# Kernel optimization log

Measured on AMD Instinct MI355X. Metric: run time of the kernel, lower is better.

The kernel has to match this reference:

```python
import jax, jax.numpy as jnp
import numpy as np

N_NODES = 100000
N_EDGES = 1600000


def gcn_conv(x, src, dst, w, W, b, n_nodes):
    # PyG GCNConv: linear -> add self-loops (weight 1) -> symmetric norm -> scatter-add -> bias
    h = x @ W  # [N, out]
    loop = jnp.arange(n_nodes, dtype=src.dtype)
    s = jnp.concatenate([src, loop])
    d = jnp.concatenate([dst, loop])
    ew = jnp.concatenate([w, jnp.ones((n_nodes,), dtype=w.dtype)])
    deg = jax.ops.segment_sum(ew, d, num_segments=n_nodes)  # weighted in-degree (incl. self-loop)
    dis = jnp.where(deg > 0, jax.lax.rsqrt(deg), 0.0)
    norm = dis[s] * ew * dis[d]  # [E+N]
    msgs = norm[:, None] * h[s]  # gather source features, scale per edge
    out = jax.ops.segment_sum(msgs, d, num_segments=n_nodes)  # scatter-add at destinations
    return out + b


def setup_inputs() -> dict:
    key = jax.random.key(0)
    ks = jax.random.split(key, 6)
    x = jax.random.normal(ks[0], (N_NODES, 128), dtype=jnp.float32)
    edge_index = jax.random.randint(ks[1], (2, N_EDGES), 0, N_NODES, dtype=jnp.int32)
    edge_weight = jax.random.uniform(ks[2], (N_EDGES,), dtype=jnp.float32)
    W1 = jax.random.normal(ks[3], (128, 64), dtype=jnp.float32) * (1.0 / np.sqrt(128))
    b1 = jnp.zeros((64,), dtype=jnp.float32)
    W2 = jax.random.normal(ks[4], (64, 16), dtype=jnp.float32) * (1.0 / np.sqrt(64))
    b2 = jnp.zeros((16,), dtype=jnp.float32)
    return {"x": x, "edge_index": edge_index, "edge_weight": edge_weight,
            "W1": W1, "b1": b1, "W2": W2, "b2": b2}


def reference(x, edge_index, edge_weight, W1, b1, W2, b2):
    src, dst = edge_index[0], edge_index[1]
    x_emb = gcn_conv(x, src, dst, edge_weight, W1, b1, N_NODES)
    h = jax.nn.relu(x_emb)  # dropout is identity in eval mode
    out = gcn_conv(h, src, dst, edge_weight, W2, b2, N_NODES)
    return (out, x_emb)
```

## Files before the change

kernel.cpp:

```cpp
#include <hip/hip_runtime.h>

#define NN 100000
#define NE 1600000
#define BSH 7
#define BSZ 128
#define NBKT 782
#define CAP 2560
#define NPB 256
#define EPB 6250

typedef unsigned short u16;
typedef unsigned int   u32;
typedef unsigned long long u64;
typedef __attribute__((ext_vector_type(8))) __bf16 bf16x8;
typedef __attribute__((ext_vector_type(4))) float  f32x4;

__device__ __forceinline__ float bf2f(u16 u) {
    union { u32 i; float f; } v; v.i = ((u32)u) << 16; return v.f;
}
__device__ __forceinline__ u16 f2bf(float f) {
    union { float f; u32 i; } v; v.f = f;
    u32 u = v.i;
    u += 0x7FFFu + ((u >> 16) & 1);
    return (u16)(u >> 16);
}
__device__ __forceinline__ float bfLO(u32 p) { return __uint_as_float(p << 16); }
__device__ __forceinline__ float bfHI(u32 p) { return __uint_as_float(p & 0xffff0000u); }
__device__ __forceinline__ u64 nt_load_u64(const uint2* p) {
    return __builtin_nontemporal_load((const u64*)p);
}

__global__ __launch_bounds__(256) void k_wpack(const float* __restrict__ W1,
                                               const float* __restrict__ W2,
                                               bf16x8* __restrict__ wp1,
                                               bf16x8* __restrict__ wp2,
                                               int* __restrict__ cursor,
                                               int* __restrict__ gctr) {
    int t = threadIdx.x;
    #pragma unroll
    for (int s = 0; s < 4; ++s) {
        int idx = s * 256 + t;
        int q = idx >> 6, l = idx & 63;
        int kb = q >> 2, ct = q & 3;
        int k0 = kb * 32 + ((l >> 4) * 8);
        int c  = ct * 16 + (l & 15);
        bf16x8 v;
        #pragma unroll
        for (int i = 0; i < 8; ++i) v[i] = (__bf16)W1[(k0 + i) * 64 + c];
        wp1[idx] = v;
    }
    if (t < 128) {
        int q = t >> 6, l = t & 63;
        int k0 = q * 32 + ((l >> 4) * 8);
        int c  = l & 15;
        bf16x8 v;
        #pragma unroll
        for (int i = 0; i < 8; ++i) v[i] = (__bf16)W2[(k0 + i) * 16 + c];
        wp2[t] = v;
    }
    for (int i = t; i < NBKT; i += 256) cursor[i] = i * CAP;
    if (t == 0) *gctr = 0;
}

__global__ __launch_bounds__(1024) void k_part(const int* __restrict__ src,
                                               const int* __restrict__ dst,
                                               const float* __restrict__ w,
                                               int* __restrict__ cursor,
                                               uint2* __restrict__ rec) {
    __shared__ uint2 sedge[EPB];
    __shared__ u16   sbkt[EPB];
    __shared__ int   cnt[NBKT];
    __shared__ int   lstart[NBKT];
    __shared__ int   gbase[NBKT];
    __shared__ int   scanbuf[1024];
    int tid = threadIdx.x;
    int e0  = blockIdx.x * EPB;

    for (int i = tid; i < NBKT; i += 1024) cnt[i] = 0;
    __syncthreads();
    for (int j = tid; j < EPB; j += 1024)
        atomicAdd(&cnt[dst[e0 + j] >> BSH], 1);
    __syncthreads();
    int v = (tid < NBKT) ? cnt[tid] : 0;
    scanbuf[tid] = v;
    __syncthreads();
    #pragma unroll
    for (int off = 1; off < 1024; off <<= 1) {
        int add = (tid >= off) ? scanbuf[tid - off] : 0;
        __syncthreads();
        scanbuf[tid] += add;
        __syncthreads();
    }
    if (tid < NBKT) lstart[tid] = scanbuf[tid] - v;
    __syncthreads();
    for (int i = tid; i < NBKT; i += 1024) {
        int c = cnt[i];
        gbase[i] = c ? atomicAdd(&cursor[i], c) : 0;
        cnt[i] = 0;
    }
    __syncthreads();
    for (int j = tid; j < EPB; j += 1024) {
        int e  = e0 + j;
        int d  = dst[e];
        int bk = d >> BSH;
        int slot = lstart[bk] + atomicAdd(&cnt[bk], 1);
        sedge[slot] = make_uint2(__float_as_uint(w[e]),
                                 ((u32)src[e] << BSH) | (u32)(d & (BSZ - 1)));
        sbkt[slot]  = (u16)bk;
    }
    __syncthreads();
    for (int j = tid; j < EPB; j += 1024) {
        int bk   = sbkt[j];
        int dest = gbase[bk] + (j - lstart[bk]);
        rec[dest] = sedge[j];
    }
}

__global__ __launch_bounds__(512) void k_build(const int* __restrict__ cursor,
                                               const uint2* __restrict__ rec,
                                               uint2* __restrict__ rec2,
                                               float* __restrict__ dis,
                                               int2* __restrict__ rowinfo,
                                               int* __restrict__ gctr) {
    __shared__ float dw[BSZ];
    __shared__ int   cnt[BSZ];
    __shared__ int   base[BSZ];
    __shared__ int   scn[BSZ];
    __shared__ float disl[BSZ];
    __shared__ int   sh_gbase;
    int b = blockIdx.x, tid = threadIdx.x;
    int s = b * CAP;
    int total = cursor[b] - s;
    if (tid < BSZ) { dw[tid] = 1.0f; cnt[tid] = 0; }
    if (tid == 0) sh_gbase = atomicAdd(gctr, total);
    __syncthreads();
    for (int j = tid; j < total; j += 512) {
        uint2 r = rec[s + j];
        int dl = r.y & (BSZ - 1);
        atomicAdd(&cnt[dl], 1);
        atomicAdd(&dw[dl], __uint_as_float(r.x));
    }
    __syncthreads();
    if (tid < BSZ) scn[tid] = cnt[tid];
    __syncthreads();
    #pragma unroll
    for (int off = 1; off < BSZ; off <<= 1) {
        int add = (tid < BSZ && tid >= off) ? scn[tid - off] : 0;
        __syncthreads();
        if (tid < BSZ) scn[tid] += add;
        __syncthreads();
    }
    int gbase = sh_gbase;
    if (tid < BSZ) {
        int node = b * BSZ + tid;
        base[tid] = (tid == 0) ? 0 : scn[tid - 1];
        float d = rsqrtf(dw[tid]);
        disl[tid] = d;
        if (node < NN) {
            dis[node] = d;
            rowinfo[node] = make_int2(gbase + base[tid], gbase + base[tid] + cnt[tid]);
        }
        cnt[tid] = 0;
    }
    __syncthreads();
    for (int j = tid; j < total; j += 512) {
        uint2 r = rec[s + j];
        int dl = r.y & (BSZ - 1);
        int pos = gbase + base[dl] + atomicAdd(&cnt[dl], 1);
        rec2[pos] = make_uint2(__float_as_uint(__uint_as_float(r.x) * disl[dl]),
                               r.y >> BSH);
    }
}

__global__ __launch_bounds__(256) void k_gemm1(const float* __restrict__ x,
                                               const bf16x8* __restrict__ wp1,
                                               const float* __restrict__ dis,
                                               u16* __restrict__ h1b) {
    int tid  = threadIdx.x;
    int lane = tid & 63;
    int wave = tid >> 6;
    int r0   = blockIdx.x * 64 + wave * 16;

    bf16x8 bfrag[16];
    #pragma unroll
    for (int q = 0; q < 16; ++q) bfrag[q] = wp1[q * 64 + lane];

    int  arow = r0 + (lane & 15);
    bool aok  = arow < NN;
    const float* xrow = x + (size_t)arow * 128 + ((lane >> 4) * 8);

    f32x4 acc0 = {0,0,0,0}, acc1 = {0,0,0,0}, acc2 = {0,0,0,0}, acc3 = {0,0,0,0};
    #pragma unroll
    for (int kb = 0; kb < 4; ++kb) {
        f32x4 xlo = {0,0,0,0}, xhi = {0,0,0,0};
        if (aok) {
            xlo = *(const f32x4*)(xrow + kb * 32);
            xhi = *(const f32x4*)(xrow + kb * 32 + 4);
        }
        bf16x8 a;
        a[0] = (__bf16)xlo[0]; a[1] = (__bf16)xlo[1]; a[2] = (__bf16)xlo[2]; a[3] = (__bf16)xlo[3];
        a[4] = (__bf16)xhi[0]; a[5] = (__bf16)xhi[1]; a[6] = (__bf16)xhi[2]; a[7] = (__bf16)xhi[3];
        acc0 = __builtin_amdgcn_mfma_f32_16x16x32_bf16(a, bfrag[kb * 4 + 0], acc0, 0, 0, 0);
        acc1 = __builtin_amdgcn_mfma_f32_16x16x32_bf16(a, bfrag[kb * 4 + 1], acc1, 0, 0, 0);
        acc2 = __builtin_amdgcn_mfma_f32_16x16x32_bf16(a, bfrag[kb * 4 + 2], acc2, 0, 0, 0);
        acc3 = __builtin_amdgcn_mfma_f32_16x16x32_bf16(a, bfrag[kb * 4 + 3], acc3, 0, 0, 0);
    }

    int rbase = r0 + (lane >> 4) * 4;
    int cbase = lane & 15;
    #pragma unroll
    for (int reg = 0; reg < 4; ++reg) {
        int row = rbase + reg;
        if (row < NN) {
            float d = dis[row];
            u16* hp = h1b + (size_t)row * 64 + cbase;
            hp[0]  = f2bf(acc0[reg] * d);
            hp[16] = f2bf(acc1[reg] * d);
            hp[32] = f2bf(acc2[reg] * d);
            hp[48] = f2bf(acc3[reg] * d);
        }
    }
}

#define ACC8(hv, nrm) { \
    a0 = fmaf(nrm, bfLO(hv.x), a0); a1 = fmaf(nrm, bfHI(hv.x), a1); \
    a2 = fmaf(nrm, bfLO(hv.y), a2); a3 = fmaf(nrm, bfHI(hv.y), a3); \
    a4 = fmaf(nrm, bfLO(hv.z), a4); a5 = fmaf(nrm, bfHI(hv.z), a5); \
    a6 = fmaf(nrm, bfLO(hv.w), a6); a7 = fmaf(nrm, bfHI(hv.w), a7); }

__global__ __launch_bounds__(512) void k_agg1(const int2* __restrict__ rowinfo,
                                              const uint2* __restrict__ rec2,
                                              const u16* __restrict__ h1b,
                                              const float* __restrict__ dis,
                                              const float* __restrict__ b1,
                                              float* __restrict__ xemb) {
    int n    = blockIdx.x * 8 + (threadIdx.x >> 6);
    int lane = threadIdx.x & 63;
    int el   = lane >> 3;
    int f8   = (lane & 7) * 8;
    int2 ri  = rowinfo[n];
    int beg = ri.x, end = ri.y;

    float a0=0,a1=0,a2=0,a3=0,a4=0,a5=0,a6=0,a7=0;

    int j0 = beg + el;
    u64 r0 = 0, r1 = 0, r2 = 0, r3 = 0;
    if (j0 < end)      r0 = nt_load_u64(&rec2[j0]);
    if (j0 + 8 < end)  r1 = nt_load_u64(&rec2[j0 + 8]);
    if (j0 + 16 < end) r2 = nt_load_u64(&rec2[j0 + 16]);
    if (j0 + 24 < end) r3 = nt_load_u64(&rec2[j0 + 24]);
    uint4 g0 = {0,0,0,0}, g1 = {0,0,0,0};
    float n0 = 0.f, n1 = 0.f;
    if (j0 < end) {
        g0 = *(const uint4*)(h1b + (size_t)(u32)(r0 >> 32) * 64 + f8);
        n0 = __uint_as_float((u32)r0);
    }
    if (j0 + 8 < end) {
        g1 = *(const uint4*)(h1b + (size_t)(u32)(r1 >> 32) * 64 + f8);
        n1 = __uint_as_float((u32)r1);
    }

    for (int j = beg; j < end; j += 16) {
        uint4 h2 = {0,0,0,0}, h3 = {0,0,0,0};
        float n2 = 0.f, n3 = 0.f;
        if (j0 + 16 < end) {
            h2 = *(const uint4*)(h1b + (size_t)(u32)(r2 >> 32) * 64 + f8);
            n2 = __uint_as_float((u32)r2);
        }
        if (j0 + 24 < end) {
            h3 = *(const uint4*)(h1b + (size_t)(u32)(r3 >> 32) * 64 + f8);
            n3 = __uint_as_float((u32)r3);
        }
        u64 nr0 = 0, nr1 = 0;
        if (j0 + 32 < end) nr0 = nt_load_u64(&rec2[j0 + 32]);
        if (j0 + 40 < end) nr1 = nt_load_u64(&rec2[j0 + 40]);
        ACC8(g0, n0);
        ACC8(g1, n1);
        g0 = h2; n0 = n2; g1 = h3; n1 = n3;
        r0 = r2; r1 = r3; r2 = nr0; r3 = nr1;
        j0 += 16;
    }

    #pragma unroll
    for (int m = 8; m <= 32; m <<= 1) {
        a0 += __shfl_xor(a0, m, 64); a1 += __shfl_xor(a1, m, 64);
        a2 += __shfl_xor(a2, m, 64); a3 += __shfl_xor(a3, m, 64);
        a4 += __shfl_xor(a4, m, 64); a5 += __shfl_xor(a5, m, 64);
        a6 += __shfl_xor(a6, m, 64); a7 += __shfl_xor(a7, m, 64);
    }
    if (el == 0) {
        float di = dis[n];
        uint4 hv = *(const uint4*)(h1b + (size_t)n * 64 + f8);
        f32x4 lo, hi;
        lo[0] = fmaf(di, bfLO(hv.x), b1[f8 + 0]) + a0;
        lo[1] = fmaf(di, bfHI(hv.x), b1[f8 + 1]) + a1;
        lo[2] = fmaf(di, bfLO(hv.y), b1[f8 + 2]) + a2;
        lo[3] = fmaf(di, bfHI(hv.y), b1[f8 + 3]) + a3;
        hi[0] = fmaf(di, bfLO(hv.z), b1[f8 + 4]) + a4;
        hi[1] = fmaf(di, bfHI(hv.z), b1[f8 + 5]) + a5;
        hi[2] = fmaf(di, bfLO(hv.w), b1[f8 + 6]) + a6;
        hi[3] = fmaf(di, bfHI(hv.w), b1[f8 + 7]) + a7;
        f32x4* dst0 = (f32x4*)&xemb[(size_t)n * 64 + f8];
        __builtin_nontemporal_store(lo, dst0);
        __builtin_nontemporal_store(hi, dst0 + 1);
    }
}

__global__ __launch_bounds__(256) void k_gemm2(const float* __restrict__ xemb,
                                               const bf16x8* __restrict__ wp2,
                                               const float* __restrict__ dis,
                                               u16* __restrict__ h3b) {
    int tid  = threadIdx.x;
    int lane = tid & 63;
    int wave = tid >> 6;
    int r0   = blockIdx.x * 64 + wave * 16;

    bf16x8 b0 = wp2[lane], b1 = wp2[64 + lane];

    int  arow = r0 + (lane & 15);
    bool aok  = arow < NN;
    const float* xrow = xemb + (size_t)arow * 64 + ((lane >> 4) * 8);

    f32x4 acc = {0,0,0,0};
    #pragma unroll
    for (int kb = 0; kb < 2; ++kb) {
        f32x4 xlo = {0,0,0,0}, xhi = {0,0,0,0};
        if (aok) {
            xlo = *(const f32x4*)(xrow + kb * 32);
            xhi = *(const f32x4*)(xrow + kb * 32 + 4);
        }
        bf16x8 a;
        #pragma unroll
        for (int i = 0; i < 4; ++i) {
            float lo = xlo[i] > 0.f ? xlo[i] : 0.f;
            float hi = xhi[i] > 0.f ? xhi[i] : 0.f;
            a[i]     = (__bf16)lo;
            a[i + 4] = (__bf16)hi;
        }
        acc = __builtin_amdgcn_mfma_f32_16x16x32_bf16(a, kb == 0 ? b0 : b1, acc, 0, 0, 0);
    }

    int rbase = r0 + (lane >> 4) * 4;
    int cbase = lane & 15;
    #pragma unroll
    for (int reg = 0; reg < 4; ++reg) {
        int row = rbase + reg;
        if (row < NN)
            h3b[(size_t)row * 16 + cbase] = f2bf(acc[reg] * dis[row]);
    }
}

__global__ __launch_bounds__(512) void k_agg2(const int2* __restrict__ rowinfo,
                                              const uint2* __restrict__ rec2,
                                              const u16* __restrict__ h3b,
                                              const float* __restrict__ dis,
                                              const float* __restrict__ b2,
                                              float* __restrict__ out) {
    int n    = blockIdx.x * 8 + (threadIdx.x >> 6);
    int lane = threadIdx.x & 63;
    int el   = lane >> 2;
    int f4   = (lane & 3) * 4;
    int2 ri  = rowinfo[n];
    int beg = ri.x, end = ri.y;

    float a0=0,a1=0,a2=0,a3=0;

    u64 p0 = 0, p1 = 0;
    if (beg + el < end)      p0 = nt_load_u64(&rec2[beg + el]);
    if (beg + 16 + el < end) p1 = nt_load_u64(&rec2[beg + 16 + el]);

    for (int j = beg; j < end; j += 32) {
        u64 q0 = 0, q1 = 0;
        if (j + 32 + el < end) q0 = nt_load_u64(&rec2[j + 32 + el]);
        if (j + 48 + el < end) q1 = nt_load_u64(&rec2[j + 48 + el]);
        if (j + el < end) {
            u32 srcn = (u32)(p0 >> 32);
            float nrm = __uint_as_float((u32)p0);
            uint2 hv = *(const uint2*)(h3b + (size_t)srcn * 16 + f4);
            a0 = fmaf(nrm, bfLO(hv.x), a0); a1 = fmaf(nrm, bfHI(hv.x), a1);
            a2 = fmaf(nrm, bfLO(hv.y), a2); a3 = fmaf(nrm, bfHI(hv.y), a3);
        }
        if (j + 16 + el < end) {
            u32 srcn = (u32)(p1 >> 32);
            float nrm = __uint_as_float((u32)p1);
            uint2 hv = *(const uint2*)(h3b + (size_t)srcn * 16 + f4);
            a0 = fmaf(nrm, bfLO(hv.x), a0); a1 = fmaf(nrm, bfHI(hv.x), a1);
            a2 = fmaf(nrm, bfLO(hv.y), a2); a3 = fmaf(nrm, bfHI(hv.y), a3);
        }
        p0 = q0; p1 = q1;
    }

    #pragma unroll
    for (int m = 4; m <= 32; m <<= 1) {
        a0 += __shfl_xor(a0, m, 64);
        a1 += __shfl_xor(a1, m, 64);
        a2 += __shfl_xor(a2, m, 64);
        a3 += __shfl_xor(a3, m, 64);
    }
    if (lane < 4) {
        float di = dis[n];
        uint2 hv = *(const uint2*)(h3b + (size_t)n * 16 + f4);
        float4 bb = *(const float4*)&b2[f4];
        float4 r;
        r.x = fmaf(di, bfLO(hv.x), bb.x) + a0;
        r.y = fmaf(di, bfHI(hv.x), bb.y) + a1;
        r.z = fmaf(di, bfLO(hv.y), bb.z) + a2;
        r.w = fmaf(di, bfHI(hv.y), bb.w) + a3;
        *(float4*)&out[(size_t)n * 16 + f4] = r;
    }
}

extern "C" void kernel_launch(void* const* d_in, const int* in_sizes, int n_in,
                              void* d_out, int out_size, void* d_ws, size_t ws_size,
                              hipStream_t stream) {
    const float* x  = (const float*)d_in[0];
    const int*   ei = (const int*)d_in[1];
    const float* w  = (const float*)d_in[2];
    const float* W1 = (const float*)d_in[3];
    const float* b1 = (const float*)d_in[4];
    const float* W2 = (const float*)d_in[5];
    const float* b2 = (const float*)d_in[6];
    const int* src = ei;
    const int* dst = ei + NE;

    float* out2 = (float*)d_out;
    float* xemb = (float*)d_out + NN * 16;

    uint2*  rec_pad = (uint2*)d_ws;
    u16*    h1b     = (u16*)d_ws;
    uint2*  rec2    = rec_pad + (size_t)NBKT * CAP;
    u16*    h3b     = (u16*)(rec2 + NE);
    bf16x8* wp1     = (bf16x8*)(h3b + (size_t)NN * 16);
    bf16x8* wp2     = wp1 + 1024;
    float*  dis     = (float*)(wp2 + 128);
    int2*   rowinfo = (int2*)(dis + NN);
    int*    cursor  = (int*)(rowinfo + NN);
    int*    gctr    = cursor + NBKT;

    k_wpack<<<1,     256, 0, stream>>>(W1, W2, wp1, wp2, cursor, gctr);
    k_part <<<NPB,  1024, 0, stream>>>(src, dst, w, cursor, rec_pad);
    k_build<<<NBKT,  512, 0, stream>>>(cursor, rec_pad, rec2, dis, rowinfo, gctr);

    k_gemm1<<<(NN + 63) / 64, 256, 0, stream>>>(x, wp1, dis, h1b);
    k_agg1 <<<NN / 8, 512, 0, stream>>>(rowinfo, rec2, h1b, dis, b1, xemb);

    k_gemm2<<<(NN + 63) / 64, 256, 0, stream>>>(xemb, wp2, dis, h3b);
    k_agg2 <<<NN / 8, 512, 0, stream>>>(rowinfo, rec2, h3b, dis, b2, out2);
}
```

Baseline: 160.1 us.

## Replace node-parallel layer-1 aggregation with edge-balanced segmented reduction

Layer-1 aggregation now gives each wave a fixed chunk of 256 CSR-ordered edges instead of giving it one destination node. Each lane owns one feature and runs a segmented sum over the chunk. Segments that span a chunk boundary are merged with atomics into an xemb buffer zeroed beforehand, and a separate kernel writes the self-loop-only value for nodes with no incoming edges. The aim is better load balance and fewer idle lanes than the per-node loop with shuffle reductions. The cost is an extra per-edge destination array, a memset, an extra kernel, and scalar 2-byte gathers per lane instead of 16-byte vector gathers.

```diff
diff --git a/kernel.cpp b/kernel.cpp
--- a/kernel.cpp
+++ b/kernel.cpp
@@ -8,6 +8,7 @@
 #define CAP 2560
 #define NPB 256
 #define EPB 6250
+#define EPW 256
 
 typedef unsigned short u16;
 typedef unsigned int   u32;
@@ -119,6 +120,7 @@
 __global__ __launch_bounds__(512) void k_build(const int* __restrict__ cursor,
                                                const uint2* __restrict__ rec,
                                                uint2* __restrict__ rec2,
+                                               u32*  __restrict__ dste,
                                                float* __restrict__ dis,
                                                int2* __restrict__ rowinfo,
                                                int* __restrict__ gctr) {
@@ -169,6 +171,7 @@
         int pos = gbase + base[dl] + atomicAdd(&cnt[dl], 1);
         rec2[pos] = make_uint2(__float_as_uint(__uint_as_float(r.x) * disl[dl]),
                                r.y >> BSH);
+        dste[pos] = (u32)(b * BSZ + dl);
     }
 }
 
@@ -222,87 +225,85 @@
     }
 }
 
-#define ACC8(hv, nrm) { \
-    a0 = fmaf(nrm, bfLO(hv.x), a0); a1 = fmaf(nrm, bfHI(hv.x), a1); \
-    a2 = fmaf(nrm, bfLO(hv.y), a2); a3 = fmaf(nrm, bfHI(hv.y), a3); \
-    a4 = fmaf(nrm, bfLO(hv.z), a4); a5 = fmaf(nrm, bfHI(hv.z), a5); \
-    a6 = fmaf(nrm, bfLO(hv.w), a6); a7 = fmaf(nrm, bfHI(hv.w), a7); }
-
-__global__ __launch_bounds__(512) void k_agg1(const int2* __restrict__ rowinfo,
-                                              const uint2* __restrict__ rec2,
+__global__ __launch_bounds__(256) void k_fix0(const int2* __restrict__ rowinfo,
                                               const u16* __restrict__ h1b,
                                               const float* __restrict__ dis,
                                               const float* __restrict__ b1,
                                               float* __restrict__ xemb) {
-    int n    = blockIdx.x * 8 + (threadIdx.x >> 6);
-    int lane = threadIdx.x & 63;
-    int el   = lane >> 3;
-    int f8   = (lane & 7) * 8;
-    int2 ri  = rowinfo[n];
-    int beg = ri.x, end = ri.y;
-
-    float a0=0,a1=0,a2=0,a3=0,a4=0,a5=0,a6=0,a7=0;
-
-    int j0 = beg + el;
-    u64 r0 = 0, r1 = 0, r2 = 0, r3 = 0;
-    if (j0 < end)      r0 = nt_load_u64(&rec2[j0]);
-    if (j0 + 8 < end)  r1 = nt_load_u64(&rec2[j0 + 8]);
-    if (j0 + 16 < end) r2 = nt_load_u64(&rec2[j0 + 16]);
-    if (j0 + 24 < end) r3 = nt_load_u64(&rec2[j0 + 24]);
-    uint4 g0 = {0,0,0,0}, g1 = {0,0,0,0};
-    float n0 = 0.f, n1 = 0.f;
-    if (j0 < end) {
-        g0 = *(const uint4*)(h1b + (size_t)(u32)(r0 >> 32) * 64 + f8);
-        n0 = __uint_as_float((u32)r0);
-    }
-    if (j0 + 8 < end) {
-        g1 = *(const uint4*)(h1b + (size_t)(u32)(r1 >> 32) * 64 + f8);
-        n1 = __uint_as_float((u32)r1);
-    }
-
-    for (int j = beg; j < end; j += 16) {
-        uint4 h2 = {0,0,0,0}, h3 = {0,0,0,0};
-        float n2 = 0.f, n3 = 0.f;
-        if (j0 + 16 < end) {
-            h2 = *(const uint4*)(h1b + (size_t)(u32)(r2 >> 32) * 64 + f8);
-            n2 = __uint_as_float((u32)r2);
-        }
-        if (j0 + 24 < end) {
-            h3 = *(const uint4*)(h1b + (size_t)(u32)(r3 >> 32) * 64 + f8);
-            n3 = __uint_as_float((u32)r3);
-        }
-        u64 nr0 = 0, nr1 = 0;
-        if (j0 + 32 < end) nr0 = nt_load_u64(&rec2[j0 + 32]);
-        if (j0 + 40 < end) nr1 = nt_load_u64(&rec2[j0 + 40]);
-        ACC8(g0, n0);
-        ACC8(g1, n1);
-        g0 = h2; n0 = n2; g1 = h3; n1 = n3;
-        r0 = r2; r1 = r3; r2 = nr0; r3 = nr1;
-        j0 += 16;
-    }
-
-    #pragma unroll
-    for (int m = 8; m <= 32; m <<= 1) {
-        a0 += __shfl_xor(a0, m, 64); a1 += __shfl_xor(a1, m, 64);
-        a2 += __shfl_xor(a2, m, 64); a3 += __shfl_xor(a3, m, 64);
-        a4 += __shfl_xor(a4, m, 64); a5 += __shfl_xor(a5, m, 64);
-        a6 += __shfl_xor(a6, m, 64); a7 += __shfl_xor(a7, m, 64);
-    }
-    if (el == 0) {
-        float di = dis[n];
-        uint4 hv = *(const uint4*)(h1b + (size_t)n * 64 + f8);
-        f32x4 lo, hi;
-        lo[0] = fmaf(di, bfLO(hv.x), b1[f8 + 0]) + a0;
-        lo[1] = fmaf(di, bfHI(hv.x), b1[f8 + 1]) + a1;
-        lo[2] = fmaf(di, bfLO(hv.y), b1[f8 + 2]) + a2;
-        lo[3] = fmaf(di, bfHI(hv.y), b1[f8 + 3]) + a3;
-        hi[0] = fmaf(di, bfLO(hv.z), b1[f8 + 4]) + a4;
-        hi[1] = fmaf(di, bfHI(hv.z), b1[f8 + 5]) + a5;
-        hi[2] = fmaf(di, bfLO(hv.w), b1[f8 + 6]) + a6;
-        hi[3] = fmaf(di, bfHI(hv.w), b1[f8 + 7]) + a7;
-        f32x4* dst0 = (f32x4*)&xemb[(size_t)n * 64 + f8];
-        __builtin_nontemporal_store(lo, dst0);
-        __builtin_nontemporal_store(hi, dst0 + 1);
+    int n = (blockIdx.x * 256 + threadIdx.x) >> 6;
+    int f = threadIdx.x & 63;
+    int2 ri = rowinfo[n];
+    if (ri.x == ri.y)
+        xemb[(size_t)n * 64 + f] = fmaf(dis[n], bf2f(h1b[(size_t)n * 64 + f]), b1[f]);
+}
+
+__global__ __launch_bounds__(512) void k_agge1(const uint2* __restrict__ rec2,
+                                               const u32* __restrict__ dste,
+                                               const u16* __restrict__ h1b,
+                                               const float* __restrict__ dis,
+                                               const float* __restrict__ b1,
+                                               float* __restrict__ xemb) {
+    int wid = blockIdx.x * 8 + (threadIdx.x >> 6);
+    if (wid >= NE / EPW) return;
+    int f  = threadIdx.x & 63;
+    int jb = wid * EPW, je = jb + EPW;
+    int pd = (jb > 0)  ? (int)dste[jb - 1] : -1;
+    int nd = (je < NE) ? (int)dste[je]     : -1;
+    float bf_ = b1[f];
+
+    u64   ru[8];
+    float pn[8];
+    u16   pv[8];
+    int   dn[8];
+    #pragma unroll
+    for (int k = 0; k < 8; ++k) {
+        u64 r = nt_load_u64(&rec2[jb + k]);
+        pn[k] = __uint_as_float((u32)r);
+        pv[k] = h1b[(size_t)(u32)(r >> 32) * 64 + f];
+        dn[k] = (int)dste[jb + k];
+        ru[k] = (jb + 8 + k < NE) ? nt_load_u64(&rec2[jb + 8 + k]) : 0;
+    }
+
+    int   curn = dn[0];
+    bool  firstseg = true;
+    float acc = 0.f;
+
+    for (int j = jb; j < je; j += 8) {
+        #pragma unroll
+        for (int k = 0; k < 8; ++k) {
+            int jj = j + k;
+            int nn = dn[k];
+            if (nn != curn) {
+                bool cont_in = firstseg && (curn == pd);
+                if (cont_in) {
+                    atomicAdd(&xemb[(size_t)curn * 64 + f], acc);
+                } else {
+                    float init = fmaf(dis[curn], bf2f(h1b[(size_t)curn * 64 + f]), bf_);
+                    xemb[(size_t)curn * 64 + f] = acc + init;
+                }
+                firstseg = false;
+                curn = nn; acc = 0.f;
+            }
+            acc = fmaf(pn[k], bf2f(pv[k]), acc);
+            int j8 = jj + 8;
+            if (j8 < je) {
+                u64 r = ru[k];
+                pn[k] = __uint_as_float((u32)r);
+                pv[k] = h1b[(size_t)(u32)(r >> 32) * 64 + f];
+                dn[k] = (int)dste[j8];
+                ru[k] = (jj + 16 < NE) ? nt_load_u64(&rec2[jj + 16]) : 0;
+            }
+        }
+    }
+    bool cont_in  = firstseg && (curn == pd);
+    bool cont_out = (curn == nd);
+    if (cont_in || cont_out) {
+        float init = cont_in ? 0.f
+                   : fmaf(dis[curn], bf2f(h1b[(size_t)curn * 64 + f]), bf_);
+        atomicAdd(&xemb[(size_t)curn * 64 + f], acc + init);
+    } else {
+        float init = fmaf(dis[curn], bf2f(h1b[(size_t)curn * 64 + f]), bf_);
+        xemb[(size_t)curn * 64 + f] = acc + init;
     }
 }
 
@@ -429,7 +430,8 @@
     uint2*  rec_pad = (uint2*)d_ws;
     u16*    h1b     = (u16*)d_ws;
     uint2*  rec2    = rec_pad + (size_t)NBKT * CAP;
-    u16*    h3b     = (u16*)(rec2 + NE);
+    u32*    dste    = (u32*)(rec2 + NE);
+    u16*    h3b     = (u16*)(dste + NE);
     bf16x8* wp1     = (bf16x8*)(h3b + (size_t)NN * 16);
     bf16x8* wp2     = wp1 + 1024;
     float*  dis     = (float*)(wp2 + 128);
@@ -439,10 +441,12 @@
 
     k_wpack<<<1,     256, 0, stream>>>(W1, W2, wp1, wp2, cursor, gctr);
     k_part <<<NPB,  1024, 0, stream>>>(src, dst, w, cursor, rec_pad);
-    k_build<<<NBKT,  512, 0, stream>>>(cursor, rec_pad, rec2, dis, rowinfo, gctr);
+    k_build<<<NBKT,  512, 0, stream>>>(cursor, rec_pad, rec2, dste, dis, rowinfo, gctr);
+    hipMemsetAsync(xemb, 0, (size_t)NN * 64 * sizeof(float), stream);
 
     k_gemm1<<<(NN + 63) / 64, 256, 0, stream>>>(x, wp1, dis, h1b);
-    k_agg1 <<<NN / 8, 512, 0, stream>>>(rowinfo, rec2, h1b, dis, b1, xemb);
+    k_fix0 <<<NN * 64 / 256, 256, 0, stream>>>(rowinfo, h1b, dis, b1, xemb);
+    k_agge1<<<(NE / EPW + 7) / 8, 512, 0, stream>>>(rec2, dste, h1b, dis, b1, xemb);
 
     k_gemm2<<<(NN + 63) / 64, 256, 0, stream>>>(xemb, wp2, dis, h3b);
     k_agg2 <<<NN / 8, 512, 0, stream>>>(rowinfo, rec2, h3b, dis, b2, out2);
```

New measurement: 363.2 us. +126.9%, slower.
